# Optimization experiments

Hardware: AMD Instinct MI355X
Metric: run time of the kernel (lower is better)

## Reference

```python
import jax, jax.numpy as jnp
import numpy as np

LOG2 = float(np.log(2.0))

def shifted_softplus(x):
    return jax.nn.softplus(x) - LOG2

def setup_inputs() -> dict:
    key = jax.random.key(0)
    ks = jax.random.split(key, 12)
    N, E = 100000, 1600000
    Cin, Cout, F_, G = 128, 128, 128, 50
    x = jax.random.normal(ks[0], (N, Cin), dtype=jnp.float32)
    edge_index = jax.random.randint(ks[1], (2, E), 0, N, dtype=jnp.int64)
    edge_attr = jax.random.uniform(ks[2], (E, G), dtype=jnp.float32)
    s = lambda fan_in: 1.0 / np.sqrt(fan_in)
    lin1_w = jax.random.uniform(ks[3], (F_, Cin), jnp.float32, -s(Cin), s(Cin))
    lin1_b = jax.random.uniform(ks[4], (F_,), jnp.float32, -s(Cin), s(Cin))
    lin2_w = jax.random.uniform(ks[5], (Cout, F_), jnp.float32, -s(F_), s(F_))
    lin2_b = jax.random.uniform(ks[6], (Cout,), jnp.float32, -s(F_), s(F_))
    fn1_w = jax.random.uniform(ks[7], (F_, G), jnp.float32, -s(G), s(G))
    fn1_b = jax.random.uniform(ks[8], (F_,), jnp.float32, -s(G), s(G))
    fn2_w = jax.random.uniform(ks[9], (F_, F_), jnp.float32, -s(F_), s(F_))
    fn2_b = jax.random.uniform(ks[10], (F_,), jnp.float32, -s(F_), s(F_))
    return {"x": x, "edge_index": edge_index, "edge_attr": edge_attr,
            "lin1_w": lin1_w, "lin1_b": lin1_b, "lin2_w": lin2_w, "lin2_b": lin2_b,
            "fn1_w": fn1_w, "fn1_b": fn1_b, "fn2_w": fn2_w, "fn2_b": fn2_b}

def reference(x, edge_index, edge_attr, lin1_w, lin1_b, lin2_w, lin2_b,
              fn1_w, fn1_b, fn2_w, fn2_b):
    row, col = edge_index[0], edge_index[1]
    # filter network: [E, G] -> [E, F]
    W = shifted_softplus(edge_attr @ fn1_w.T + fn1_b) @ fn2_w.T + fn2_b
    # transform nodes then gather source features: [E, F]
    x_j = (x @ lin1_w.T + lin1_b)[col]
    msg = x_j * W
    # scatter-add over destination nodes: [N, F]
    agg = jax.ops.segment_sum(msg, row, num_segments=x.shape[0])
    return agg @ lin2_w.T + lin2_b
```

## Files before the change

kernel.cpp:

```cpp
#include <hip/hip_runtime.h>

#define NN 100000
#define NE 1600000
#define CC 128
#define GG 50
#define EPB 128
#define NSCB 98

typedef _Float16 half8 __attribute__((ext_vector_type(8)));
typedef float f32x4 __attribute__((ext_vector_type(4)));

static __device__ __forceinline__ f32x4 mfma16(half8 a, half8 b, f32x4 c) {
    return __builtin_amdgcn_mfma_f32_16x16x32_f16(a, b, c, 0, 0, 0);
}

__global__ __launch_bounds__(256) void pack_frags(const float* fn1_w, const float* fn2_w,
                                                  _Float16* ws_frag)
{
    int tid = threadIdx.x;
    for (int s = tid; s < 1024; s += 256) {
        int l = s & 63, ks = (s >> 6) & 1, nb = s >> 7;
        int f = nb * 16 + (l & 15);
        int k0 = ks * 32 + 8 * (l >> 4);
        half8 v;
        #pragma unroll
        for (int i = 0; i < 8; i++) {
            int g = k0 + i;
            v[i] = (g < GG) ? (_Float16)fn1_w[f * GG + g] : (_Float16)0.f;
        }
        *reinterpret_cast<half8*>(&ws_frag[s * 8]) = v;
    }
    for (int s = tid; s < 2048; s += 256) {
        int l = s & 63, ks = (s >> 6) & 3, nb = s >> 8;
        int f = nb * 16 + (l & 15);
        int k0 = ks * 32 + 8 * (l >> 4);
        const float* wp = fn2_w + f * CC + k0;
        half8 v;
        #pragma unroll
        for (int i = 0; i < 8; i++) v[i] = (_Float16)wp[i];
        *reinterpret_cast<half8*>(&ws_frag[8192 + s * 8]) = v;
    }
}

template <typename OutT>
__global__ __launch_bounds__(256) void lin_kernel(const float* in, const float* w,
                                                  const float* bias, OutT* out, int nrows)
{
    __shared__ __align__(16) _Float16 a_lds[64][136];
    __shared__ __align__(16) _Float16 bfrag[2048 * 8];

    int tid = threadIdx.x;
    int rowBase = blockIdx.x * 64;

    for (int i = tid; i < 64 * 32; i += 256) {
        int r = i >> 5, c4 = i & 31;
        float4 v = {0.f, 0.f, 0.f, 0.f};
        if (rowBase + r < nrows)
            v = reinterpret_cast<const float4*>(in)[(size_t)(rowBase + r) * (CC / 4) + c4];
        a_lds[r][c4 * 4 + 0] = (_Float16)v.x;
        a_lds[r][c4 * 4 + 1] = (_Float16)v.y;
        a_lds[r][c4 * 4 + 2] = (_Float16)v.z;
        a_lds[r][c4 * 4 + 3] = (_Float16)v.w;
    }
    for (int s = tid; s < 2048; s += 256) {
        int l = s & 63, ks = (s >> 6) & 3, nb = s >> 8;
        int f = nb * 16 + (l & 15);
        int k0 = ks * 32 + 8 * (l >> 4);
        const float* wp = w + f * CC + k0;
        half8 v;
        #pragma unroll
        for (int i = 0; i < 8; i++) v[i] = (_Float16)wp[i];
        *reinterpret_cast<half8*>(&bfrag[s * 8]) = v;
    }
    __syncthreads();

    int wid = tid >> 6, l = tid & 63;
    int lr = l & 15, lg = l >> 4;
    int wrow = wid * 16;

    half8 afr[4];
    #pragma unroll
    for (int ks = 0; ks < 4; ks++)
        afr[ks] = *reinterpret_cast<const half8*>(&a_lds[wrow + lr][ks * 32 + 8 * lg]);

    #pragma unroll
    for (int nb = 0; nb < 8; nb++) {
        f32x4 acc = {0.f, 0.f, 0.f, 0.f};
        #pragma unroll
        for (int ks = 0; ks < 4; ks++) {
            half8 bf = *reinterpret_cast<const half8*>(&bfrag[((nb * 4 + ks) * 64 + l) * 8]);
            acc = mfma16(afr[ks], bf, acc);
        }
        float bv = bias[nb * 16 + lr];
        #pragma unroll
        for (int j = 0; j < 4; j++) {
            int r = rowBase + wrow + lg * 4 + j;
            if (r < nrows) out[(size_t)r * CC + nb * 16 + lr] = (OutT)(acc[j] + bv);
        }
    }
}

__global__ __launch_bounds__(256) void hist_kernel(const int* row, int* cnt) {
    int e = blockIdx.x * 256 + threadIdx.x;
    if (e < NE) atomicAdd(&cnt[row[e]], 1);
}

__global__ __launch_bounds__(256) void scanA(const int* cnt, int* excl, int* bsum) {
    __shared__ int lds[256];
    int b = blockIdx.x, t = threadIdx.x;
    int base = b * 1024 + t * 4;
    int v[4];
    #pragma unroll
    for (int i = 0; i < 4; i++) v[i] = (base + i < NN) ? cnt[base + i] : 0;
    int s = v[0] + v[1] + v[2] + v[3];
    lds[t] = s;
    __syncthreads();
    for (int off = 1; off < 256; off <<= 1) {
        int x = (t >= off) ? lds[t - off] : 0;
        __syncthreads();
        lds[t] += x;
        __syncthreads();
    }
    int incl = lds[t];
    int run = incl - s;
    #pragma unroll
    for (int i = 0; i < 4; i++) {
        if (base + i < NN) excl[base + i] = run;
        run += v[i];
    }
    if (t == 255) bsum[b] = incl;
}

__global__ __launch_bounds__(128) void scanB(int* bsum) {
    __shared__ int lds[128];
    int t = threadIdx.x;
    int v = (t < NSCB) ? bsum[t] : 0;
    lds[t] = v;
    __syncthreads();
    for (int off = 1; off < 128; off <<= 1) {
        int x = (t >= off) ? lds[t - off] : 0;
        __syncthreads();
        lds[t] += x;
        __syncthreads();
    }
    if (t < NSCB) bsum[t] = lds[t] - v;
}

__global__ __launch_bounds__(256) void scanC(int* excl, const int* bsum) {
    int b = blockIdx.x, t = threadIdx.x;
    int off = bsum[b];
    int base = b * 1024 + t * 4;
    #pragma unroll
    for (int i = 0; i < 4; i++)
        if (base + i < NN) excl[base + i] += off;
}

__global__ __launch_bounds__(256) void build_perm(const int* row, int* cursor, int* perm) {
    int e = blockIdx.x * 256 + threadIdx.x;
    if (e < NE) {
        int r = row[e];
        int p = atomicAdd(&cursor[r], 1);
        perm[p] = e;
    }
}

__global__ __launch_bounds__(512, 8) void edge_kernel_sorted(
    const _Float16* __restrict__ x1, const int* __restrict__ eidx,
    const float* __restrict__ ea, const _Float16* __restrict__ frag_ws,
    const float* __restrict__ fn1_b, const float* __restrict__ fn2_b,
    const int* __restrict__ perm, float* __restrict__ agg)
{
    __shared__ __align__(16) unsigned char u_lds[EPB * CC * 2];
    __shared__ int pe_l[EPB];
    __shared__ int row_l[EPB];
    __shared__ int col_l[EPB];

    int tid = threadIdx.x;
    size_t eBase = (size_t)blockIdx.x * EPB;

    if (tid < EPB) pe_l[tid] = perm[eBase + tid];
    __syncthreads();

    if (tid < EPB) {
        int pe = pe_l[tid];
        row_l[tid] = eidx[pe];
        col_l[tid] = eidx[(size_t)NE + pe];
    }
    {
        int i = tid >> 2, p = tid & 3;
        int pe = pe_l[i];
        const float2* src = reinterpret_cast<const float2*>(ea + (size_t)pe * GG);
        int swz = (i & 7) << 4;
        #pragma unroll
        for (int it = 0; it < 7; it++) {
            int g2 = p + it * 4;
            if (g2 < 25) {
                float2 v = src[g2];
                int byte = i * 128 + ((g2 * 4) ^ swz);
                _Float16* q = reinterpret_cast<_Float16*>(u_lds + byte);
                q[0] = (_Float16)v.x;
                q[1] = (_Float16)v.y;
            }
        }
        #pragma unroll
        for (int it = 0; it < 2; it++) {
            int g2 = 25 + p + it * 4;
            if (g2 < 32) {
                int byte = i * 128 + ((g2 * 4) ^ swz);
                _Float16* q = reinterpret_cast<_Float16*>(u_lds + byte);
                q[0] = (_Float16)0.f;
                q[1] = (_Float16)0.f;
            }
        }
    }
    __syncthreads();

    int w = tid >> 6, l = tid & 63;
    int lr = l & 15, lg = l >> 4;
    int erow = w * 16;

    half8 a1[2];
    #pragma unroll
    for (int ks = 0; ks < 2; ks++) {
        int e = erow + lr;
        int byte = e * 128 + ((ks * 64 + lg * 16) ^ ((e & 7) << 4));
        a1[ks] = *reinterpret_cast<const half8*>(u_lds + byte);
    }
    __syncthreads();

    #pragma unroll
    for (int nb = 0; nb < 8; nb++) {
        half8 b10 = *reinterpret_cast<const half8*>(&frag_ws[((nb * 2 + 0) * 64 + l) * 8]);
        half8 b11 = *reinterpret_cast<const half8*>(&frag_ws[((nb * 2 + 1) * 64 + l) * 8]);
        f32x4 acc = {0.f, 0.f, 0.f, 0.f};
        acc = mfma16(a1[0], b10, acc);
        acc = mfma16(a1[1], b11, acc);
        float bv = fn1_b[nb * 16 + lr];
        int f = nb * 16 + lr;
        #pragma unroll
        for (int j = 0; j < 4; j++) {
            float z = acc[j] + bv;
            float t = __expf(-fabsf(z));
            float h = fmaxf(z, 0.f) + __logf(1.f + t) - 0.69314718055994531f;
            int e = erow + lg * 4 + j;
            int byte = e * 256 + ((f * 2) ^ ((e & 7) << 4));
            *reinterpret_cast<_Float16*>(u_lds + byte) = (_Float16)h;
        }
    }
    __syncthreads();

    half8 a2[4];
    #pragma unroll
    for (int ks = 0; ks < 4; ks++) {
        int e = erow + lr;
        int byte = e * 256 + ((ks * 64 + lg * 16) ^ ((e & 7) << 4));
        a2[ks] = *reinterpret_cast<const half8*>(u_lds + byte);
    }

    int cc4[4];
    #pragma unroll
    for (int j = 0; j < 4; j++) cc4[j] = col_l[erow + lg * 4 + j];

    const half8* b2g = reinterpret_cast<const half8*>(frag_ws + 8192);
    #pragma unroll
    for (int nb = 0; nb < 8; nb++) {
        f32x4 acc = {0.f, 0.f, 0.f, 0.f};
        #pragma unroll
        for (int ks = 0; ks < 4; ks++) {
            half8 bf = b2g[(nb * 4 + ks) * 64 + l];
            acc = mfma16(a2[ks], bf, acc);
        }
        float bv = fn2_b[nb * 16 + lr];
        int f = nb * 16 + lr;
        #pragma unroll
        for (int j = 0; j < 4; j++) {
            int e = erow + lg * 4 + j;
            float wv = acc[j] + bv;
            float xv = (float)x1[(size_t)cc4[j] * CC + f];
            int byte = e * 256 + ((f * 2) ^ ((e & 7) << 4));
            *reinterpret_cast<_Float16*>(u_lds + byte) = (_Float16)(xv * wv);
        }
    }
    __syncthreads();

    {
        int f = tid & 127;
        int c0 = (tid >> 7) * 32;
        float acc = 0.f;
        int cur = row_l[c0];
        for (int k = 0; k < 32; k++) {
            int e = c0 + k;
            int r = row_l[e];
            if (r != cur) {
                atomicAdd(&agg[(size_t)cur * CC + f], acc);
                acc = 0.f;
                cur = r;
            }
            int byte = e * 256 + ((f * 2) ^ ((e & 7) << 4));
            acc += (float)*reinterpret_cast<const _Float16*>(u_lds + byte);
        }
        atomicAdd(&agg[(size_t)cur * CC + f], acc);
    }
}

__global__ __launch_bounds__(512, 8) void edge_kernel_atomic(
    const _Float16* __restrict__ x1, const int* __restrict__ eidx,
    const float* __restrict__ ea, const _Float16* __restrict__ frag_ws,
    const float* __restrict__ fn1_b, const float* __restrict__ fn2_b,
    float* __restrict__ agg)
{
    __shared__ __align__(16) unsigned char u_lds[EPB * CC * 2];
    __shared__ int rows_l[EPB];
    __shared__ int cols_l[EPB];

    int tid = threadIdx.x;
    size_t eBase = (size_t)blockIdx.x * EPB;

    if (tid < EPB) {
        rows_l[tid] = eidx[eBase + tid];
        cols_l[tid] = eidx[(size_t)NE + eBase + tid];
    }
    {
        const float2* eap = reinterpret_cast<const float2*>(ea + eBase * GG);
        for (int i = tid; i < EPB * 25; i += 512) {
            int e = i / 25, g2 = i - e * 25;
            float2 v = eap[i];
            int byte = e * 128 + ((g2 * 4) ^ ((e & 7) << 4));
            _Float16* p = reinterpret_cast<_Float16*>(u_lds + byte);
            p[0] = (_Float16)v.x;
            p[1] = (_Float16)v.y;
        }
        for (int i = tid; i < EPB * 14; i += 512) {
            int e = i / 14, g = (i - e * 14) + 50;
            int byte = e * 128 + ((g * 2) ^ ((e & 7) << 4));
            *reinterpret_cast<_Float16*>(u_lds + byte) = (_Float16)0.f;
        }
    }
    __syncthreads();

    int w = tid >> 6, l = tid & 63;
    int lr = l & 15, lg = l >> 4;
    int erow = w * 16;

    half8 a1[2];
    #pragma unroll
    for (int ks = 0; ks < 2; ks++) {
        int e = erow + lr;
        int byte = e * 128 + ((ks * 64 + lg * 16) ^ ((e & 7) << 4));
        a1[ks] = *reinterpret_cast<const half8*>(u_lds + byte);
    }
    __syncthreads();

    #pragma unroll
    for (int nb = 0; nb < 8; nb++) {
        half8 b10 = *reinterpret_cast<const half8*>(&frag_ws[((nb * 2 + 0) * 64 + l) * 8]);
        half8 b11 = *reinterpret_cast<const half8*>(&frag_ws[((nb * 2 + 1) * 64 + l) * 8]);
        f32x4 acc = {0.f, 0.f, 0.f, 0.f};
        acc = mfma16(a1[0], b10, acc);
        acc = mfma16(a1[1], b11, acc);
        float bv = fn1_b[nb * 16 + lr];
        int f = nb * 16 + lr;
        #pragma unroll
        for (int j = 0; j < 4; j++) {
            float z = acc[j] + bv;
            float t = __expf(-fabsf(z));
            float h = fmaxf(z, 0.f) + __logf(1.f + t) - 0.69314718055994531f;
            int e = erow + lg * 4 + j;
            int byte = e * 256 + ((f * 2) ^ ((e & 7) << 4));
            *reinterpret_cast<_Float16*>(u_lds + byte) = (_Float16)h;
        }
    }
    __syncthreads();

    half8 a2[4];
    #pragma unroll
    for (int ks = 0; ks < 4; ks++) {
        int e = erow + lr;
        int byte = e * 256 + ((ks * 64 + lg * 16) ^ ((e & 7) << 4));
        a2[ks] = *reinterpret_cast<const half8*>(u_lds + byte);
    }

    int rr[4], cc4[4];
    #pragma unroll
    for (int j = 0; j < 4; j++) {
        int e = erow + lg * 4 + j;
        rr[j] = rows_l[e];
        cc4[j] = cols_l[e];
    }

    const half8* b2g = reinterpret_cast<const half8*>(frag_ws + 8192);
    #pragma unroll
    for (int nb = 0; nb < 8; nb++) {
        f32x4 acc = {0.f, 0.f, 0.f, 0.f};
        #pragma unroll
        for (int ks = 0; ks < 4; ks++) {
            half8 bf = b2g[(nb * 4 + ks) * 64 + l];
            acc = mfma16(a2[ks], bf, acc);
        }
        float bv = fn2_b[nb * 16 + lr];
        int f = nb * 16 + lr;
        #pragma unroll
        for (int j = 0; j < 4; j++) {
            float wv = acc[j] + bv;
            float xv = (float)x1[(size_t)cc4[j] * CC + f];
            atomicAdd(&agg[(size_t)rr[j] * CC + f], xv * wv);
        }
    }
}

extern "C" void kernel_launch(void* const* d_in, const int* in_sizes, int n_in,
                              void* d_out, int out_size, void* d_ws, size_t ws_size,
                              hipStream_t stream) {
    const float* x      = (const float*)d_in[0];
    const int*   eidx   = (const int*)d_in[1];
    const float* ea     = (const float*)d_in[2];
    const float* lin1_w = (const float*)d_in[3];
    const float* lin1_b = (const float*)d_in[4];
    const float* lin2_w = (const float*)d_in[5];
    const float* lin2_b = (const float*)d_in[6];
    const float* fn1_w  = (const float*)d_in[7];
    const float* fn1_b  = (const float*)d_in[8];
    const float* fn2_w  = (const float*)d_in[9];
    const float* fn2_b  = (const float*)d_in[10];

    float* out = (float*)d_out;
    float* agg = out;

    const size_t o_frag   = 0;
    const size_t o_x1h    = 65536;
    const size_t o_perm   = o_x1h + (size_t)NN * CC * 2;
    const size_t o_rowptr = o_perm + (size_t)NE * 4;
    const size_t o_bsum   = o_rowptr + (size_t)(NN + 1) * 4 + 60;
    const size_t o_cnt    = o_bsum + 1024;
    const size_t req      = o_cnt + (size_t)NN * 4;

    _Float16* frag_ws = (_Float16*)((char*)d_ws + o_frag);
    _Float16* x1h     = (_Float16*)((char*)d_ws + o_x1h);

    hipMemsetAsync(agg, 0, (size_t)NN * CC * sizeof(float), stream);
    pack_frags<<<1, 256, 0, stream>>>(fn1_w, fn2_w, frag_ws);
    lin_kernel<_Float16><<<(NN + 63) / 64, 256, 0, stream>>>(x, lin1_w, lin1_b, x1h, NN);

    if (ws_size >= req) {
        int* perm   = (int*)((char*)d_ws + o_perm);
        int* rowptr = (int*)((char*)d_ws + o_rowptr);
        int* bsum   = (int*)((char*)d_ws + o_bsum);
        int* cnt    = (int*)((char*)d_ws + o_cnt);

        hipMemsetAsync(cnt, 0, (size_t)NN * 4, stream);
        hist_kernel<<<(NE + 255) / 256, 256, 0, stream>>>(eidx, cnt);
        scanA<<<NSCB, 256, 0, stream>>>(cnt, rowptr, bsum);
        scanB<<<1, 128, 0, stream>>>(bsum);
        scanC<<<NSCB, 256, 0, stream>>>(rowptr, bsum);
        build_perm<<<(NE + 255) / 256, 256, 0, stream>>>(eidx, rowptr, perm);

        edge_kernel_sorted<<<NE / EPB, 512, 0, stream>>>(x1h, eidx, ea, frag_ws,
                                                         fn1_b, fn2_b, perm, agg);
    } else {
        edge_kernel_atomic<<<NE / EPB, 512, 0, stream>>>(x1h, eidx, ea, frag_ws,
                                                         fn1_b, fn2_b, agg);
    }

    lin_kernel<float><<<(NN + 63) / 64, 256, 0, stream>>>(agg, lin2_w, lin2_b, out, NN);
}
```

Before: 784.7 us.

## Replace atomic scatter with owner-block segmented writes over stable-sorted edges

Edges are now sorted by destination with a sub-key on the edge-index chunk, so ordering within each row is approximately stable. The sort uses 8x more histogram bins plus a row-pointer array. In the edge kernel, the block that owns a row's start writes aggregates directly instead of using atomics. The block holding the last row also walks forward through later tiles to finish that row, which removes float atomics and makes results deterministic. The trade-off is extra sort work and possible serial tail recomputation for long rows, because those trailing tiles are computed twice.

```diff
diff --git a/kernel.cpp b/kernel.cpp
--- a/kernel.cpp
+++ b/kernel.cpp
@@ -5,7 +5,9 @@
 #define CC 128
 #define GG 50
 #define EPB 128
-#define NSCB 98
+#define KSH 18
+#define NSORT (NN * 8)
+#define NSCB2 782
 
 typedef _Float16 half8 __attribute__((ext_vector_type(8)));
 typedef float f32x4 __attribute__((ext_vector_type(4)));
@@ -102,16 +104,20 @@
 
 __global__ __launch_bounds__(256) void hist_kernel(const int* row, int* cnt) {
     int e = blockIdx.x * 256 + threadIdx.x;
-    if (e < NE) atomicAdd(&cnt[row[e]], 1);
-}
-
-__global__ __launch_bounds__(256) void scanA(const int* cnt, int* excl, int* bsum) {
+    if (e < NE) {
+        int r = row[e];
+        int k = e >> KSH;
+        atomicAdd(&cnt[r * 8 + k], 1);
+    }
+}
+
+__global__ __launch_bounds__(256) void scanA(const int* cnt, int* excl, int* bsum, int n) {
     __shared__ int lds[256];
     int b = blockIdx.x, t = threadIdx.x;
     int base = b * 1024 + t * 4;
     int v[4];
     #pragma unroll
-    for (int i = 0; i < 4; i++) v[i] = (base + i < NN) ? cnt[base + i] : 0;
+    for (int i = 0; i < 4; i++) v[i] = (base + i < n) ? cnt[base + i] : 0;
     int s = v[0] + v[1] + v[2] + v[3];
     lds[t] = s;
     __syncthreads();
@@ -125,70 +131,150 @@
     int run = incl - s;
     #pragma unroll
     for (int i = 0; i < 4; i++) {
-        if (base + i < NN) excl[base + i] = run;
+        if (base + i < n) excl[base + i] = run;
         run += v[i];
     }
     if (t == 255) bsum[b] = incl;
 }
 
-__global__ __launch_bounds__(128) void scanB(int* bsum) {
-    __shared__ int lds[128];
+__global__ __launch_bounds__(256) void scanB(int* bsum, int n) {
+    __shared__ int lds[256];
     int t = threadIdx.x;
-    int v = (t < NSCB) ? bsum[t] : 0;
-    lds[t] = v;
-    __syncthreads();
-    for (int off = 1; off < 128; off <<= 1) {
+    int base = t * 4;
+    int v[4];
+    #pragma unroll
+    for (int i = 0; i < 4; i++) v[i] = (base + i < n) ? bsum[base + i] : 0;
+    int s = v[0] + v[1] + v[2] + v[3];
+    lds[t] = s;
+    __syncthreads();
+    for (int off = 1; off < 256; off <<= 1) {
         int x = (t >= off) ? lds[t - off] : 0;
         __syncthreads();
         lds[t] += x;
         __syncthreads();
     }
-    if (t < NSCB) bsum[t] = lds[t] - v;
-}
-
-__global__ __launch_bounds__(256) void scanC(int* excl, const int* bsum) {
+    int run = lds[t] - s;
+    #pragma unroll
+    for (int i = 0; i < 4; i++) {
+        if (base + i < n) bsum[base + i] = run;
+        run += v[i];
+    }
+}
+
+__global__ __launch_bounds__(256) void scanC(int* excl, const int* bsum, int* rowptr2, int n) {
     int b = blockIdx.x, t = threadIdx.x;
     int off = bsum[b];
     int base = b * 1024 + t * 4;
     #pragma unroll
-    for (int i = 0; i < 4; i++)
-        if (base + i < NN) excl[base + i] += off;
+    for (int i = 0; i < 4; i++) {
+        int idx = base + i;
+        if (idx < n) {
+            int val = excl[idx] + off;
+            excl[idx] = val;
+            if ((idx & 7) == 0) rowptr2[idx >> 3] = val;
+        }
+    }
 }
 
 __global__ __launch_bounds__(256) void build_perm(const int* row, int* cursor, int* perm) {
     int e = blockIdx.x * 256 + threadIdx.x;
     if (e < NE) {
         int r = row[e];
-        int p = atomicAdd(&cursor[r], 1);
+        int k = e >> KSH;
+        int p = atomicAdd(&cursor[r * 8 + k], 1);
         perm[p] = e;
     }
 }
 
-__global__ __launch_bounds__(512, 8) void edge_kernel_sorted(
-    const _Float16* __restrict__ x1, const int* __restrict__ eidx,
-    const float* __restrict__ ea, const _Float16* __restrict__ frag_ws,
+__device__ __forceinline__ void tile_compute(
+    unsigned char* u_lds, const int* col_l,
+    const _Float16* __restrict__ frag_ws,
     const float* __restrict__ fn1_b, const float* __restrict__ fn2_b,
-    const int* __restrict__ perm, float* __restrict__ agg)
+    const _Float16* __restrict__ x1, int tid, int nAct)
 {
-    __shared__ __align__(16) unsigned char u_lds[EPB * CC * 2];
-    __shared__ int pe_l[EPB];
-    __shared__ int row_l[EPB];
-    __shared__ int col_l[EPB];
-
-    int tid = threadIdx.x;
-    size_t eBase = (size_t)blockIdx.x * EPB;
-
-    if (tid < EPB) pe_l[tid] = perm[eBase + tid];
-    __syncthreads();
-
-    if (tid < EPB) {
-        int pe = pe_l[tid];
-        row_l[tid] = eidx[pe];
-        col_l[tid] = eidx[(size_t)NE + pe];
-    }
-    {
-        int i = tid >> 2, p = tid & 3;
-        int pe = pe_l[i];
+    int l = tid & 63, w = tid >> 6;
+    int lr = l & 15, lg = l >> 4;
+    int erow = w * 16;
+    bool act = erow < nAct;
+
+    half8 a1[2];
+    if (act) {
+        #pragma unroll
+        for (int ks = 0; ks < 2; ks++) {
+            int e = erow + lr;
+            int byte = e * 128 + ((ks * 64 + lg * 16) ^ ((e & 7) << 4));
+            a1[ks] = *reinterpret_cast<const half8*>(u_lds + byte);
+        }
+    }
+    __syncthreads();
+
+    if (act) {
+        #pragma unroll
+        for (int nb = 0; nb < 8; nb++) {
+            half8 b10 = *reinterpret_cast<const half8*>(&frag_ws[((nb * 2 + 0) * 64 + l) * 8]);
+            half8 b11 = *reinterpret_cast<const half8*>(&frag_ws[((nb * 2 + 1) * 64 + l) * 8]);
+            f32x4 acc = {0.f, 0.f, 0.f, 0.f};
+            acc = mfma16(a1[0], b10, acc);
+            acc = mfma16(a1[1], b11, acc);
+            float bv = fn1_b[nb * 16 + lr];
+            int f = nb * 16 + lr;
+            #pragma unroll
+            for (int j = 0; j < 4; j++) {
+                float z = acc[j] + bv;
+                float t = __expf(-fabsf(z));
+                float h = fmaxf(z, 0.f) + __logf(1.f + t) - 0.69314718055994531f;
+                int e = erow + lg * 4 + j;
+                int byte = e * 256 + ((f * 2) ^ ((e & 7) << 4));
+                *reinterpret_cast<_Float16*>(u_lds + byte) = (_Float16)h;
+            }
+        }
+    }
+    __syncthreads();
+
+    if (act) {
+        half8 a2[4];
+        #pragma unroll
+        for (int ks = 0; ks < 4; ks++) {
+            int e = erow + lr;
+            int byte = e * 256 + ((ks * 64 + lg * 16) ^ ((e & 7) << 4));
+            a2[ks] = *reinterpret_cast<const half8*>(u_lds + byte);
+        }
+        int cc4[4];
+        #pragma unroll
+        for (int j = 0; j < 4; j++) cc4[j] = col_l[erow + lg * 4 + j];
+
+        const half8* b2g = reinterpret_cast<const half8*>(frag_ws + 8192);
+        #pragma unroll
+        for (int nb = 0; nb < 8; nb++) {
+            f32x4 acc = {0.f, 0.f, 0.f, 0.f};
+            #pragma unroll
+            for (int ks = 0; ks < 4; ks++) {
+                half8 bf = b2g[(nb * 4 + ks) * 64 + l];
+                acc = mfma16(a2[ks], bf, acc);
+            }
+            float bv = fn2_b[nb * 16 + lr];
+            int f = nb * 16 + lr;
+            #pragma unroll
+            for (int j = 0; j < 4; j++) {
+                int e = erow + lg * 4 + j;
+                float wv = acc[j] + bv;
+                float xv = (float)x1[(size_t)cc4[j] * CC + f];
+                int byte = e * 256 + ((f * 2) ^ ((e & 7) << 4));
+                *reinterpret_cast<_Float16*>(u_lds + byte) = (_Float16)(xv * wv);
+            }
+        }
+    }
+}
+
+__device__ __forceinline__ void gather_tile(
+    unsigned char* u_lds, int* col_l, const int* __restrict__ perm,
+    const int* __restrict__ eidx, const float* __restrict__ ea,
+    int tid, int src0, int nAct)
+{
+    int i = tid >> 2, p = tid & 3;
+    if (i < nAct) {
+        int pe = perm[src0 + i];
+        if (p == 0) col_l[i] = eidx[(size_t)NE + pe];
         const float2* src = reinterpret_cast<const float2*>(ea + (size_t)pe * GG);
         int swz = (i & 7) << 4;
         #pragma unroll
@@ -213,94 +299,105 @@
             }
         }
     }
-    __syncthreads();
-
-    int w = tid >> 6, l = tid & 63;
-    int lr = l & 15, lg = l >> 4;
-    int erow = w * 16;
-
-    half8 a1[2];
-    #pragma unroll
-    for (int ks = 0; ks < 2; ks++) {
-        int e = erow + lr;
-        int byte = e * 128 + ((ks * 64 + lg * 16) ^ ((e & 7) << 4));
-        a1[ks] = *reinterpret_cast<const half8*>(u_lds + byte);
-    }
-    __syncthreads();
-
-    #pragma unroll
-    for (int nb = 0; nb < 8; nb++) {
-        half8 b10 = *reinterpret_cast<const half8*>(&frag_ws[((nb * 2 + 0) * 64 + l) * 8]);
-        half8 b11 = *reinterpret_cast<const half8*>(&frag_ws[((nb * 2 + 1) * 64 + l) * 8]);
-        f32x4 acc = {0.f, 0.f, 0.f, 0.f};
-        acc = mfma16(a1[0], b10, acc);
-        acc = mfma16(a1[1], b11, acc);
-        float bv = fn1_b[nb * 16 + lr];
-        int f = nb * 16 + lr;
-        #pragma unroll
-        for (int j = 0; j < 4; j++) {
-            float z = acc[j] + bv;
-            float t = __expf(-fabsf(z));
-            float h = fmaxf(z, 0.f) + __logf(1.f + t) - 0.69314718055994531f;
-            int e = erow + lg * 4 + j;
-            int byte = e * 256 + ((f * 2) ^ ((e & 7) << 4));
-            *reinterpret_cast<_Float16*>(u_lds + byte) = (_Float16)h;
-        }
-    }
-    __syncthreads();
-
-    half8 a2[4];
-    #pragma unroll
-    for (int ks = 0; ks < 4; ks++) {
-        int e = erow + lr;
-        int byte = e * 256 + ((ks * 64 + lg * 16) ^ ((e & 7) << 4));
-        a2[ks] = *reinterpret_cast<const half8*>(u_lds + byte);
-    }
-
-    int cc4[4];
-    #pragma unroll
-    for (int j = 0; j < 4; j++) cc4[j] = col_l[erow + lg * 4 + j];
-
-    const half8* b2g = reinterpret_cast<const half8*>(frag_ws + 8192);
-    #pragma unroll
-    for (int nb = 0; nb < 8; nb++) {
-        f32x4 acc = {0.f, 0.f, 0.f, 0.f};
-        #pragma unroll
-        for (int ks = 0; ks < 4; ks++) {
-            half8 bf = b2g[(nb * 4 + ks) * 64 + l];
-            acc = mfma16(a2[ks], bf, acc);
-        }
-        float bv = fn2_b[nb * 16 + lr];
-        int f = nb * 16 + lr;
-        #pragma unroll
-        for (int j = 0; j < 4; j++) {
-            int e = erow + lg * 4 + j;
-            float wv = acc[j] + bv;
-            float xv = (float)x1[(size_t)cc4[j] * CC + f];
-            int byte = e * 256 + ((f * 2) ^ ((e & 7) << 4));
-            *reinterpret_cast<_Float16*>(u_lds + byte) = (_Float16)(xv * wv);
-        }
-    }
-    __syncthreads();
-
+}
+
+__global__ __launch_bounds__(512, 8) void edge_kernel_owner(
+    const _Float16* __restrict__ x1, const int* __restrict__ eidx,
+    const float* __restrict__ ea, const _Float16* __restrict__ frag_ws,
+    const float* __restrict__ fn1_b, const float* __restrict__ fn2_b,
+    const int* __restrict__ perm, const int* __restrict__ rowptr2,
+    float* __restrict__ agg)
+{
+    __shared__ __align__(16) unsigned char u_lds[EPB * CC * 2];
+    __shared__ int pe_l[EPB];
+    __shared__ int row_l[EPB];
+    __shared__ int col_l[EPB];
+
+    int tid = threadIdx.x;
+    int base = blockIdx.x * EPB;
+
+    if (tid < EPB) pe_l[tid] = perm[base + tid];
+    __syncthreads();
+    if (tid < EPB) {
+        int pe = pe_l[tid];
+        row_l[tid] = eidx[pe];
+        col_l[tid] = eidx[(size_t)NE + pe];
+    }
     {
-        int f = tid & 127;
-        int c0 = (tid >> 7) * 32;
+        int i = tid >> 2, p = tid & 3;
+        int pe = pe_l[i];
+        const float2* src = reinterpret_cast<const float2*>(ea + (size_t)pe * GG);
+        int swz = (i & 7) << 4;
+        #pragma unroll
+        for (int it = 0; it < 7; it++) {
+            int g2 = p + it * 4;
+            if (g2 < 25) {
+                float2 v = src[g2];
+                int byte = i * 128 + ((g2 * 4) ^ swz);
+                _Float16* q = reinterpret_cast<_Float16*>(u_lds + byte);
+                q[0] = (_Float16)v.x;
+                q[1] = (_Float16)v.y;
+            }
+        }
+        #pragma unroll
+        for (int it = 0; it < 2; it++) {
+            int g2 = 25 + p + it * 4;
+            if (g2 < 32) {
+                int byte = i * 128 + ((g2 * 4) ^ swz);
+                _Float16* q = reinterpret_cast<_Float16*>(u_lds + byte);
+                q[0] = (_Float16)0.f;
+                q[1] = (_Float16)0.f;
+            }
+        }
+    }
+    __syncthreads();
+
+    int r0 = row_l[0];
+    int rl = row_l[EPB - 1];
+    bool owned0 = (rowptr2[r0] == base);
+    bool ownedL = (rowptr2[rl] >= base);
+    int endLast = (rl + 1 < NN) ? rowptr2[rl + 1] : NE;
+
+    tile_compute(u_lds, col_l, frag_ws, fn1_b, fn2_b, x1, tid, EPB);
+    __syncthreads();
+
+    float lastAcc = 0.f;
+    if (tid < 128) {
+        int f = tid;
         float acc = 0.f;
-        int cur = row_l[c0];
-        for (int k = 0; k < 32; k++) {
-            int e = c0 + k;
-            int r = row_l[e];
+        int cur = row_l[0];
+        bool firstRun = true;
+        for (int i = 0; i < EPB; i++) {
+            int r = row_l[i];
             if (r != cur) {
-                atomicAdd(&agg[(size_t)cur * CC + f], acc);
+                if (!firstRun || owned0) agg[(size_t)cur * CC + f] = acc;
+                firstRun = false;
                 acc = 0.f;
                 cur = r;
             }
-            int byte = e * 256 + ((f * 2) ^ ((e & 7) << 4));
+            int byte = i * 256 + ((f * 2) ^ ((i & 7) << 4));
             acc += (float)*reinterpret_cast<const _Float16*>(u_lds + byte);
         }
-        atomicAdd(&agg[(size_t)cur * CC + f], acc);
-    }
+        lastAcc = acc;
+    }
+
+    for (int t0 = base + EPB; ownedL && t0 < endLast; t0 += EPB) {
+        int S = endLast - t0;
+        if (S > EPB) S = EPB;
+        __syncthreads();
+        gather_tile(u_lds, col_l, perm, eidx, ea, tid, t0, S);
+        __syncthreads();
+        tile_compute(u_lds, col_l, frag_ws, fn1_b, fn2_b, x1, tid, S);
+        __syncthreads();
+        if (tid < 128) {
+            int f = tid;
+            for (int k = 0; k < S; k++) {
+                int byte = k * 256 + ((f * 2) ^ ((k & 7) << 4));
+                lastAcc += (float)*reinterpret_cast<const _Float16*>(u_lds + byte);
+            }
+        }
+    }
+    if (ownedL && tid < 128) agg[(size_t)rl * CC + tid] = lastAcc;
 }
 
 __global__ __launch_bounds__(512, 8) void edge_kernel_atomic(
@@ -338,72 +435,21 @@
     }
     __syncthreads();
 
+    tile_compute(u_lds, cols_l, frag_ws, fn1_b, fn2_b, x1, tid, EPB);
+    __syncthreads();
+
     int w = tid >> 6, l = tid & 63;
     int lr = l & 15, lg = l >> 4;
     int erow = w * 16;
-
-    half8 a1[2];
-    #pragma unroll
-    for (int ks = 0; ks < 2; ks++) {
-        int e = erow + lr;
-        int byte = e * 128 + ((ks * 64 + lg * 16) ^ ((e & 7) << 4));
-        a1[ks] = *reinterpret_cast<const half8*>(u_lds + byte);
-    }
-    __syncthreads();
-
     #pragma unroll
     for (int nb = 0; nb < 8; nb++) {
-        half8 b10 = *reinterpret_cast<const half8*>(&frag_ws[((nb * 2 + 0) * 64 + l) * 8]);
-        half8 b11 = *reinterpret_cast<const half8*>(&frag_ws[((nb * 2 + 1) * 64 + l) * 8]);
-        f32x4 acc = {0.f, 0.f, 0.f, 0.f};
-        acc = mfma16(a1[0], b10, acc);
-        acc = mfma16(a1[1], b11, acc);
-        float bv = fn1_b[nb * 16 + lr];
         int f = nb * 16 + lr;
         #pragma unroll
         for (int j = 0; j < 4; j++) {
-            float z = acc[j] + bv;
-            float t = __expf(-fabsf(z));
-            float h = fmaxf(z, 0.f) + __logf(1.f + t) - 0.69314718055994531f;
             int e = erow + lg * 4 + j;
             int byte = e * 256 + ((f * 2) ^ ((e & 7) << 4));
-            *reinterpret_cast<_Float16*>(u_lds + byte) = (_Float16)h;
-        }
-    }
-    __syncthreads();
-
-    half8 a2[4];
-    #pragma unroll
-    for (int ks = 0; ks < 4; ks++) {
-        int e = erow + lr;
-        int byte = e * 256 + ((ks * 64 + lg * 16) ^ ((e & 7) << 4));
-        a2[ks] = *reinterpret_cast<const half8*>(u_lds + byte);
-    }
-
-    int rr[4], cc4[4];
-    #pragma unroll
-    for (int j = 0; j < 4; j++) {
-        int e = erow + lg * 4 + j;
-        rr[j] = rows_l[e];
-        cc4[j] = cols_l[e];
-    }
-
-    const half8* b2g = reinterpret_cast<const half8*>(frag_ws + 8192);
-    #pragma unroll
-    for (int nb = 0; nb < 8; nb++) {
-        f32x4 acc = {0.f, 0.f, 0.f, 0.f};
-        #pragma unroll
-        for (int ks = 0; ks < 4; ks++) {
-            half8 bf = b2g[(nb * 4 + ks) * 64 + l];
-            acc = mfma16(a2[ks], bf, acc);
-        }
-        float bv = fn2_b[nb * 16 + lr];
-        int f = nb * 16 + lr;
-        #pragma unroll
-        for (int j = 0; j < 4; j++) {
-            float wv = acc[j] + bv;
-            float xv = (float)x1[(size_t)cc4[j] * CC + f];
-            atomicAdd(&agg[(size_t)rr[j] * CC + f], xv * wv);
+            float mv = (float)*reinterpret_cast<const _Float16*>(u_lds + byte);
+            atomicAdd(&agg[(size_t)rows_l[e] * CC + f], mv);
         }
     }
 }
@@ -426,13 +472,13 @@
     float* out = (float*)d_out;
     float* agg = out;
 
-    const size_t o_frag   = 0;
-    const size_t o_x1h    = 65536;
-    const size_t o_perm   = o_x1h + (size_t)NN * CC * 2;
-    const size_t o_rowptr = o_perm + (size_t)NE * 4;
-    const size_t o_bsum   = o_rowptr + (size_t)(NN + 1) * 4 + 60;
-    const size_t o_cnt    = o_bsum + 1024;
-    const size_t req      = o_cnt + (size_t)NN * 4;
+    const size_t o_frag = 0;
+    const size_t o_x1h  = 65536;
+    const size_t o_perm = o_x1h + (size_t)NN * CC * 2;
+    const size_t o_cur  = o_perm + (size_t)NE * 4;
+    const size_t o_rp2  = o_cur + (size_t)NSORT * 4;
+    const size_t o_bsum = o_rp2 + (size_t)NN * 4;
+    const size_t req    = o_bsum + 4096;
 
     _Float16* frag_ws = (_Float16*)((char*)d_ws + o_frag);
     _Float16* x1h     = (_Float16*)((char*)d_ws + o_x1h);
@@ -442,20 +488,20 @@
     lin_kernel<_Float16><<<(NN + 63) / 64, 256, 0, stream>>>(x, lin1_w, lin1_b, x1h, NN);
 
     if (ws_size >= req) {
-        int* perm   = (int*)((char*)d_ws + o_perm);
-        int* rowptr = (int*)((char*)d_ws + o_rowptr);
-        int* bsum   = (int*)((char*)d_ws + o_bsum);
-        int* cnt    = (int*)((char*)d_ws + o_cnt);
-
-        hipMemsetAsync(cnt, 0, (size_t)NN * 4, stream);
-        hist_kernel<<<(NE + 255) / 256, 256, 0, stream>>>(eidx, cnt);
-        scanA<<<NSCB, 256, 0, stream>>>(cnt, rowptr, bsum);
-        scanB<<<1, 128, 0, stream>>>(bsum);
-        scanC<<<NSCB, 256, 0, stream>>>(rowptr, bsum);
-        build_perm<<<(NE + 255) / 256, 256, 0, stream>>>(eidx, rowptr, perm);
-
-        edge_kernel_sorted<<<NE / EPB, 512, 0, stream>>>(x1h, eidx, ea, frag_ws,
-                                                         fn1_b, fn2_b, perm, agg);
+        int* perm    = (int*)((char*)d_ws + o_perm);
+        int* cursor  = (int*)((char*)d_ws + o_cur);
+        int* rowptr2 = (int*)((char*)d_ws + o_rp2);
+        int* bsum    = (int*)((char*)d_ws + o_bsum);
+
+        hipMemsetAsync(cursor, 0, (size_t)NSORT * 4, stream);
+        hist_kernel<<<(NE + 255) / 256, 256, 0, stream>>>(eidx, cursor);
+        scanA<<<NSCB2, 256, 0, stream>>>(cursor, cursor, bsum, NSORT);
+        scanB<<<1, 256, 0, stream>>>(bsum, NSCB2);
+        scanC<<<NSCB2, 256, 0, stream>>>(cursor, bsum, rowptr2, NSORT);
+        build_perm<<<(NE + 255) / 256, 256, 0, stream>>>(eidx, cursor, perm);
+
+        edge_kernel_owner<<<NE / EPB, 512, 0, stream>>>(x1h, eidx, ea, frag_ws,
+                                                        fn1_b, fn2_b, perm, rowptr2, agg);
     } else {
         edge_kernel_atomic<<<NE / EPB, 512, 0, stream>>>(x1h, eidx, ea, frag_ws,
                                                          fn1_b, fn2_b, agg);
```

Result: slower. 1.805 ms (+130.1%).

## Replace sorted-gather edge kernel with message scatter plus segmented gather-reduce

Applied to the files above, without the earlier changes.

Edges are now processed in their original order, so edge_attr and edge_index reads are coalesced instead of going through a permutation. Each edge's fp16 message is written to its destination-sorted slot, taken from a per-row cursor atomic. A separate per-node kernel then sums each row's contiguous messages without float atomics and feeds an fp16 aggregate into the output linear layer. This drops build_perm, the agg memset and the global atomics, but adds an edge-sized fp16 message buffer of hundreds of MB that must be written and read back. It also raises the workspace requirement a lot, and if the workspace is too small the slow atomic path runs instead.

```diff
diff --git a/kernel.cpp b/kernel.cpp
--- a/kernel.cpp
+++ b/kernel.cpp
@@ -8,6 +8,7 @@
 #define NSCB 98
 
 typedef _Float16 half8 __attribute__((ext_vector_type(8)));
+typedef _Float16 half2v __attribute__((ext_vector_type(2)));
 typedef float f32x4 __attribute__((ext_vector_type(4)));
 
 static __device__ __forceinline__ f32x4 mfma16(half8 a, half8 b, f32x4 c) {
@@ -42,8 +43,8 @@
     }
 }
 
-template <typename OutT>
-__global__ __launch_bounds__(256) void lin_kernel(const float* in, const float* w,
+template <typename InT, typename OutT>
+__global__ __launch_bounds__(256) void lin_kernel(const InT* in, const float* w,
                                                   const float* bias, OutT* out, int nrows)
 {
     __shared__ __align__(16) _Float16 a_lds[64][136];
@@ -52,15 +53,27 @@
     int tid = threadIdx.x;
     int rowBase = blockIdx.x * 64;
 
-    for (int i = tid; i < 64 * 32; i += 256) {
-        int r = i >> 5, c4 = i & 31;
-        float4 v = {0.f, 0.f, 0.f, 0.f};
-        if (rowBase + r < nrows)
-            v = reinterpret_cast<const float4*>(in)[(size_t)(rowBase + r) * (CC / 4) + c4];
-        a_lds[r][c4 * 4 + 0] = (_Float16)v.x;
-        a_lds[r][c4 * 4 + 1] = (_Float16)v.y;
-        a_lds[r][c4 * 4 + 2] = (_Float16)v.z;
-        a_lds[r][c4 * 4 + 3] = (_Float16)v.w;
+    if constexpr (sizeof(InT) == 4) {
+        for (int i = tid; i < 64 * 32; i += 256) {
+            int r = i >> 5, c4 = i & 31;
+            float4 v = {0.f, 0.f, 0.f, 0.f};
+            if (rowBase + r < nrows)
+                v = reinterpret_cast<const float4*>(in)[(size_t)(rowBase + r) * (CC / 4) + c4];
+            a_lds[r][c4 * 4 + 0] = (_Float16)v.x;
+            a_lds[r][c4 * 4 + 1] = (_Float16)v.y;
+            a_lds[r][c4 * 4 + 2] = (_Float16)v.z;
+            a_lds[r][c4 * 4 + 3] = (_Float16)v.w;
+        }
+    } else {
+        for (int i = tid; i < 64 * 16; i += 256) {
+            int r = i >> 4, c8 = i & 15;
+            half8 v;
+            #pragma unroll
+            for (int k = 0; k < 8; k++) v[k] = (_Float16)0.f;
+            if (rowBase + r < nrows)
+                v = reinterpret_cast<const half8*>(in)[(size_t)(rowBase + r) * (CC / 8) + c8];
+            *reinterpret_cast<half8*>(&a_lds[r][c8 * 8]) = v;
+        }
     }
     for (int s = tid; s < 2048; s += 256) {
         int l = s & 63, ks = (s >> 6) & 3, nb = s >> 8;
@@ -105,13 +118,13 @@
     if (e < NE) atomicAdd(&cnt[row[e]], 1);
 }
 
-__global__ __launch_bounds__(256) void scanA(const int* cnt, int* excl, int* bsum) {
+__global__ __launch_bounds__(256) void scanA(const int* cnt, int* excl, int* bsum, int n) {
     __shared__ int lds[256];
     int b = blockIdx.x, t = threadIdx.x;
     int base = b * 1024 + t * 4;
     int v[4];
     #pragma unroll
-    for (int i = 0; i < 4; i++) v[i] = (base + i < NN) ? cnt[base + i] : 0;
+    for (int i = 0; i < 4; i++) v[i] = (base + i < n) ? cnt[base + i] : 0;
     int s = v[0] + v[1] + v[2] + v[3];
     lds[t] = s;
     __syncthreads();
@@ -125,16 +138,16 @@
     int run = incl - s;
     #pragma unroll
     for (int i = 0; i < 4; i++) {
-        if (base + i < NN) excl[base + i] = run;
+        if (base + i < n) excl[base + i] = run;
         run += v[i];
     }
     if (t == 255) bsum[b] = incl;
 }
 
-__global__ __launch_bounds__(128) void scanB(int* bsum) {
+__global__ __launch_bounds__(128) void scanB(int* bsum, int n) {
     __shared__ int lds[128];
     int t = threadIdx.x;
-    int v = (t < NSCB) ? bsum[t] : 0;
+    int v = (t < n) ? bsum[t] : 0;
     lds[t] = v;
     __syncthreads();
     for (int off = 1; off < 128; off <<= 1) {
@@ -143,81 +156,65 @@
         lds[t] += x;
         __syncthreads();
     }
-    if (t < NSCB) bsum[t] = lds[t] - v;
-}
-
-__global__ __launch_bounds__(256) void scanC(int* excl, const int* bsum) {
+    if (t < n) bsum[t] = lds[t] - v;
+}
+
+__global__ __launch_bounds__(256) void scanC(int* excl, const int* bsum, int* cursor, int n) {
     int b = blockIdx.x, t = threadIdx.x;
     int off = bsum[b];
     int base = b * 1024 + t * 4;
     #pragma unroll
-    for (int i = 0; i < 4; i++)
-        if (base + i < NN) excl[base + i] += off;
-}
-
-__global__ __launch_bounds__(256) void build_perm(const int* row, int* cursor, int* perm) {
-    int e = blockIdx.x * 256 + threadIdx.x;
-    if (e < NE) {
-        int r = row[e];
-        int p = atomicAdd(&cursor[r], 1);
-        perm[p] = e;
-    }
-}
-
-__global__ __launch_bounds__(512, 8) void edge_kernel_sorted(
+    for (int i = 0; i < 4; i++) {
+        int idx = base + i;
+        if (idx < n) {
+            int val = excl[idx] + off;
+            excl[idx] = val;
+            cursor[idx] = val;
+        }
+    }
+}
+
+__global__ __launch_bounds__(512, 8) void msg_scatter_kernel(
     const _Float16* __restrict__ x1, const int* __restrict__ eidx,
     const float* __restrict__ ea, const _Float16* __restrict__ frag_ws,
     const float* __restrict__ fn1_b, const float* __restrict__ fn2_b,
-    const int* __restrict__ perm, float* __restrict__ agg)
+    int* __restrict__ cursor, _Float16* __restrict__ msg)
 {
     __shared__ __align__(16) unsigned char u_lds[EPB * CC * 2];
-    __shared__ int pe_l[EPB];
-    __shared__ int row_l[EPB];
-    __shared__ int col_l[EPB];
+    __shared__ int rows_l[EPB];
+    __shared__ int cols_l[EPB];
+    __shared__ int p_l[EPB];
 
     int tid = threadIdx.x;
     size_t eBase = (size_t)blockIdx.x * EPB;
 
-    if (tid < EPB) pe_l[tid] = perm[eBase + tid];
-    __syncthreads();
-
     if (tid < EPB) {
-        int pe = pe_l[tid];
-        row_l[tid] = eidx[pe];
-        col_l[tid] = eidx[(size_t)NE + pe];
+        rows_l[tid] = eidx[eBase + tid];
+        cols_l[tid] = eidx[(size_t)NE + eBase + tid];
     }
     {
-        int i = tid >> 2, p = tid & 3;
-        int pe = pe_l[i];
-        const float2* src = reinterpret_cast<const float2*>(ea + (size_t)pe * GG);
-        int swz = (i & 7) << 4;
-        #pragma unroll
-        for (int it = 0; it < 7; it++) {
-            int g2 = p + it * 4;
-            if (g2 < 25) {
-                float2 v = src[g2];
-                int byte = i * 128 + ((g2 * 4) ^ swz);
-                _Float16* q = reinterpret_cast<_Float16*>(u_lds + byte);
-                q[0] = (_Float16)v.x;
-                q[1] = (_Float16)v.y;
-            }
-        }
-        #pragma unroll
-        for (int it = 0; it < 2; it++) {
-            int g2 = 25 + p + it * 4;
-            if (g2 < 32) {
-                int byte = i * 128 + ((g2 * 4) ^ swz);
-                _Float16* q = reinterpret_cast<_Float16*>(u_lds + byte);
-                q[0] = (_Float16)0.f;
-                q[1] = (_Float16)0.f;
-            }
-        }
-    }
-    __syncthreads();
-
-    int w = tid >> 6, l = tid & 63;
+        const float2* eap = reinterpret_cast<const float2*>(ea + eBase * GG);
+        for (int i = tid; i < EPB * 25; i += 512) {
+            int e = i / 25, g2 = i - e * 25;
+            float2 v = eap[i];
+            int byte = e * 128 + ((g2 * 4) ^ ((e & 7) << 4));
+            _Float16* p = reinterpret_cast<_Float16*>(u_lds + byte);
+            p[0] = (_Float16)v.x;
+            p[1] = (_Float16)v.y;
+        }
+        for (int i = tid; i < EPB * 14; i += 512) {
+            int e = i / 14, g = (i - e * 14) + 50;
+            int byte = e * 128 + ((g * 2) ^ ((e & 7) << 4));
+            *reinterpret_cast<_Float16*>(u_lds + byte) = (_Float16)0.f;
+        }
+    }
+    __syncthreads();
+
+    if (tid < EPB) p_l[tid] = atomicAdd(&cursor[rows_l[tid]], 1);
+
+    int wv = tid >> 6, l = tid & 63;
     int lr = l & 15, lg = l >> 4;
-    int erow = w * 16;
+    int erow = wv * 16;
 
     half8 a1[2];
     #pragma unroll
@@ -241,10 +238,10 @@
         for (int j = 0; j < 4; j++) {
             float z = acc[j] + bv;
             float t = __expf(-fabsf(z));
-            float h = fmaxf(z, 0.f) + __logf(1.f + t) - 0.69314718055994531f;
+            float hz = fmaxf(z, 0.f) + __logf(1.f + t) - 0.69314718055994531f;
             int e = erow + lg * 4 + j;
             int byte = e * 256 + ((f * 2) ^ ((e & 7) << 4));
-            *reinterpret_cast<_Float16*>(u_lds + byte) = (_Float16)h;
+            *reinterpret_cast<_Float16*>(u_lds + byte) = (_Float16)hz;
         }
     }
     __syncthreads();
@@ -256,10 +253,9 @@
         int byte = e * 256 + ((ks * 64 + lg * 16) ^ ((e & 7) << 4));
         a2[ks] = *reinterpret_cast<const half8*>(u_lds + byte);
     }
-
     int cc4[4];
     #pragma unroll
-    for (int j = 0; j < 4; j++) cc4[j] = col_l[erow + lg * 4 + j];
+    for (int j = 0; j < 4; j++) cc4[j] = cols_l[erow + lg * 4 + j];
 
     const half8* b2g = reinterpret_cast<const half8*>(frag_ws + 8192);
     #pragma unroll
@@ -275,32 +271,57 @@
         #pragma unroll
         for (int j = 0; j < 4; j++) {
             int e = erow + lg * 4 + j;
-            float wv = acc[j] + bv;
+            float wvv = acc[j] + bv;
             float xv = (float)x1[(size_t)cc4[j] * CC + f];
             int byte = e * 256 + ((f * 2) ^ ((e & 7) << 4));
-            *reinterpret_cast<_Float16*>(u_lds + byte) = (_Float16)(xv * wv);
+            *reinterpret_cast<_Float16*>(u_lds + byte) = (_Float16)(xv * wvv);
         }
     }
     __syncthreads();
 
     {
-        int f = tid & 127;
-        int c0 = (tid >> 7) * 32;
-        float acc = 0.f;
-        int cur = row_l[c0];
-        for (int k = 0; k < 32; k++) {
-            int e = c0 + k;
-            int r = row_l[e];
-            if (r != cur) {
-                atomicAdd(&agg[(size_t)cur * CC + f], acc);
-                acc = 0.f;
-                cur = r;
-            }
-            int byte = e * 256 + ((f * 2) ^ ((e & 7) << 4));
-            acc += (float)*reinterpret_cast<const _Float16*>(u_lds + byte);
-        }
-        atomicAdd(&agg[(size_t)cur * CC + f], acc);
-    }
+        int i = tid >> 2, part = tid & 3;
+        int swz = (i & 7) << 4;
+        size_t dst = (size_t)p_l[i] * CC + part * 32;
+        #pragma unroll
+        for (int q = 0; q < 4; q++) {
+            int byte = i * 256 + ((part * 64 + q * 16) ^ swz);
+            float4 v = *reinterpret_cast<const float4*>(u_lds + byte);
+            *reinterpret_cast<float4*>(&msg[dst + q * 8]) = v;
+        }
+    }
+}
+
+__global__ __launch_bounds__(512, 8) void gather_reduce_kernel(
+    const _Float16* __restrict__ msg, const int* __restrict__ rowptr,
+    _Float16* __restrict__ aggH)
+{
+    int tid = threadIdx.x;
+    int r = blockIdx.x * 8 + (tid >> 6);
+    int l = tid & 63;
+    int e0 = rowptr[r];
+    int e1 = (r == NN - 1) ? NE : rowptr[r + 1];
+
+    const unsigned* base = reinterpret_cast<const unsigned*>(msg) + l;
+    float a0 = 0.f, a1 = 0.f;
+    int i = e0;
+    for (; i + 1 < e1; i += 2) {
+        unsigned v0 = base[(size_t)i * 64];
+        unsigned v1 = base[(size_t)(i + 1) * 64];
+        half2v h0 = __builtin_bit_cast(half2v, v0);
+        half2v h1 = __builtin_bit_cast(half2v, v1);
+        a0 += (float)h0[0] + (float)h1[0];
+        a1 += (float)h0[1] + (float)h1[1];
+    }
+    if (i < e1) {
+        half2v h = __builtin_bit_cast(half2v, base[(size_t)i * 64]);
+        a0 += (float)h[0];
+        a1 += (float)h[1];
+    }
+    half2v o;
+    o[0] = (_Float16)a0;
+    o[1] = (_Float16)a1;
+    reinterpret_cast<unsigned*>(aggH)[(size_t)r * 64 + l] = __builtin_bit_cast(unsigned, o);
 }
 
 __global__ __launch_bounds__(512, 8) void edge_kernel_atomic(
@@ -338,9 +359,9 @@
     }
     __syncthreads();
 
-    int w = tid >> 6, l = tid & 63;
+    int wv = tid >> 6, l = tid & 63;
     int lr = l & 15, lg = l >> 4;
-    int erow = w * 16;
+    int erow = wv * 16;
 
     half8 a1[2];
     #pragma unroll
@@ -364,10 +385,10 @@
         for (int j = 0; j < 4; j++) {
             float z = acc[j] + bv;
             float t = __expf(-fabsf(z));
-            float h = fmaxf(z, 0.f) + __logf(1.f + t) - 0.69314718055994531f;
+            float hz = fmaxf(z, 0.f) + __logf(1.f + t) - 0.69314718055994531f;
             int e = erow + lg * 4 + j;
             int byte = e * 256 + ((f * 2) ^ ((e & 7) << 4));
-            *reinterpret_cast<_Float16*>(u_lds + byte) = (_Float16)h;
+            *reinterpret_cast<_Float16*>(u_lds + byte) = (_Float16)hz;
         }
     }
     __syncthreads();
@@ -379,7 +400,6 @@
         int byte = e * 256 + ((ks * 64 + lg * 16) ^ ((e & 7) << 4));
         a2[ks] = *reinterpret_cast<const half8*>(u_lds + byte);
     }
-
     int rr[4], cc4[4];
     #pragma unroll
     for (int j = 0; j < 4; j++) {
@@ -387,7 +407,6 @@
         rr[j] = rows_l[e];
         cc4[j] = cols_l[e];
     }
-
     const half8* b2g = reinterpret_cast<const half8*>(frag_ws + 8192);
     #pragma unroll
     for (int nb = 0; nb < 8; nb++) {
@@ -401,9 +420,9 @@
         int f = nb * 16 + lr;
         #pragma unroll
         for (int j = 0; j < 4; j++) {
-            float wv = acc[j] + bv;
+            float wvv = acc[j] + bv;
             float xv = (float)x1[(size_t)cc4[j] * CC + f];
-            atomicAdd(&agg[(size_t)rr[j] * CC + f], xv * wv);
+            atomicAdd(&agg[(size_t)rr[j] * CC + f], xv * wvv);
         }
     }
 }
@@ -424,42 +443,45 @@
     const float* fn2_b  = (const float*)d_in[10];
 
     float* out = (float*)d_out;
-    float* agg = out;
-
-    const size_t o_frag   = 0;
-    const size_t o_x1h    = 65536;
-    const size_t o_perm   = o_x1h + (size_t)NN * CC * 2;
-    const size_t o_rowptr = o_perm + (size_t)NE * 4;
-    const size_t o_bsum   = o_rowptr + (size_t)(NN + 1) * 4 + 60;
-    const size_t o_cnt    = o_bsum + 1024;
-    const size_t req      = o_cnt + (size_t)NN * 4;
+
+    const size_t o_frag = 0;
+    const size_t o_x1h  = 65536;
+    const size_t o_msg  = o_x1h + (size_t)NN * CC * 2;
+    const size_t o_aggH = o_msg + (size_t)NE * CC * 2;
+    const size_t o_cnt  = o_aggH + (size_t)NN * CC * 2;
+    const size_t o_rp   = o_cnt + (size_t)NN * 4;
+    const size_t o_cur  = o_rp + (size_t)NN * 4;
+    const size_t o_bsum = o_cur + (size_t)NN * 4;
+    const size_t req    = o_bsum + 512;
 
     _Float16* frag_ws = (_Float16*)((char*)d_ws + o_frag);
     _Float16* x1h     = (_Float16*)((char*)d_ws + o_x1h);
 
-    hipMemsetAsync(agg, 0, (size_t)NN * CC * sizeof(float), stream);
     pack_frags<<<1, 256, 0, stream>>>(fn1_w, fn2_w, frag_ws);
-    lin_kernel<_Float16><<<(NN + 63) / 64, 256, 0, stream>>>(x, lin1_w, lin1_b, x1h, NN);
+    lin_kernel<float, _Float16><<<(NN + 63) / 64, 256, 0, stream>>>(x, lin1_w, lin1_b, x1h, NN);
 
     if (ws_size >= req) {
-        int* perm   = (int*)((char*)d_ws + o_perm);
-        int* rowptr = (int*)((char*)d_ws + o_rowptr);
+        _Float16* msg  = (_Float16*)((char*)d_ws + o_msg);
+        _Float16* aggH = (_Float16*)((char*)d_ws + o_aggH);
+        int* cnt    = (int*)((char*)d_ws + o_cnt);
+        int* rowptr = (int*)((char*)d_ws + o_rp);
+        int* cursor = (int*)((char*)d_ws + o_cur);
         int* bsum   = (int*)((char*)d_ws + o_bsum);
-        int* cnt    = (int*)((char*)d_ws + o_cnt);
 
         hipMemsetAsync(cnt, 0, (size_t)NN * 4, stream);
         hist_kernel<<<(NE + 255) / 256, 256, 0, stream>>>(eidx, cnt);
-        scanA<<<NSCB, 256, 0, stream>>>(cnt, rowptr, bsum);
-        scanB<<<1, 128, 0, stream>>>(bsum);
-        scanC<<<NSCB, 256, 0, stream>>>(rowptr, bsum);
-        build_perm<<<(NE + 255) / 256, 256, 0, stream>>>(eidx, rowptr, perm);
-
-        edge_kernel_sorted<<<NE / EPB, 512, 0, stream>>>(x1h, eidx, ea, frag_ws,
-                                                         fn1_b, fn2_b, perm, agg);
+        scanA<<<NSCB, 256, 0, stream>>>(cnt, rowptr, bsum, NN);
+        scanB<<<1, 128, 0, stream>>>(bsum, NSCB);
+        scanC<<<NSCB, 256, 0, stream>>>(rowptr, bsum, cursor, NN);
+
+        msg_scatter_kernel<<<NE / EPB, 512, 0, stream>>>(x1h, eidx, ea, frag_ws,
+                                                         fn1_b, fn2_b, cursor, msg);
+        gather_reduce_kernel<<<NN / 8, 512, 0, stream>>>(msg, rowptr, aggH);
+        lin_kernel<_Float16, float><<<(NN + 63) / 64, 256, 0, stream>>>(aggH, lin2_w, lin2_b, out, NN);
     } else {
+        hipMemsetAsync(out, 0, (size_t)NN * CC * sizeof(float), stream);
         edge_kernel_atomic<<<NE / EPB, 512, 0, stream>>>(x1h, eidx, ea, frag_ws,
-                                                         fn1_b, fn2_b, agg);
-    }
-
-    lin_kernel<float><<<(NN + 63) / 64, 256, 0, stream>>>(agg, lin2_w, lin2_b, out, NN);
-}
+                                                         fn1_b, fn2_b, out);
+        lin_kernel<float, float><<<(NN + 63) / 64, 256, 0, stream>>>(out, lin2_w, lin2_b, out, NN);
+    }
+}
```

Measured after the change: 834.7 us. +6.4%, slower.
